# Kernel optimization log

Hardware: AMD Instinct MI355X
Metric: run time of the kernel (lower is better)

The kernel has to match this reference:

```python
import jax, jax.numpy as jnp
import numpy as np
import math

B, S, D, H = 2, 2048, 1024, 16
DH = D // H
EPS = 1e-5
GELU_C = 0.7978845608

def setup_inputs() -> dict:
    key = jax.random.key(0)
    ks = jax.random.split(key, 8)
    s = 0.02
    return {
        "x": jax.random.normal(ks[0], (B, S, D), jnp.float32),
        "gamma1": jnp.ones((D,), jnp.float32),
        "beta1": jnp.zeros((D,), jnp.float32),
        "W_qkv": jax.random.normal(ks[1], (D, 3 * D), jnp.float32) * s,
        "b_qkv": jnp.zeros((3 * D,), jnp.float32),
        "W_o": jax.random.normal(ks[2], (D, D), jnp.float32) * s,
        "b_o": jnp.zeros((D,), jnp.float32),
        "gamma2": jnp.ones((D,), jnp.float32),
        "beta2": jnp.zeros((D,), jnp.float32),
        "W_up": jax.random.normal(ks[3], (D, 4 * D), jnp.float32) * s,
        "b_up": jnp.zeros((4 * D,), jnp.float32),
        "W_down": jax.random.normal(ks[4], (4 * D, D), jnp.float32) * s,
        "b_down": jnp.zeros((D,), jnp.float32),
    }

def _layernorm(x, gamma, beta):
    # Matches the torch module: unbiased std (ddof=1), eps added to std.
    mean = jnp.mean(x, axis=-1, keepdims=True)
    std = jnp.std(x, axis=-1, keepdims=True, ddof=1)
    return gamma * (x - mean) / (std + EPS) + beta

def _gelu(x):
    return 0.5 * x * (1.0 + jnp.tanh(GELU_C * (x + 0.044715 * x * x * x)))

def reference(x, gamma1, beta1, W_qkv, b_qkv, W_o, b_o, gamma2, beta2, W_up, b_up, W_down, b_down):
    b, s, _ = x.shape
    # --- attention branch ---
    h = _layernorm(x, gamma1, beta1)
    qkv = (h @ W_qkv + b_qkv).reshape(b, s, H, 3, DH)
    q, k, v = qkv[..., 0, :], qkv[..., 1, :], qkv[..., 2, :]  # [b,s,h,dh]
    scores = jnp.einsum("bqhd,bkhd->bhqk", q, k) / math.sqrt(DH)
    causal = jnp.tril(jnp.ones((s, s), bool))
    scores = jnp.where(causal, scores, -jnp.inf)
    attn = jax.nn.softmax(scores, axis=-1)
    o = jnp.einsum("bhqk,bkhd->bqhd", attn, v).reshape(b, s, D)
    attn_out = o @ W_o + b_o + x
    # --- mlp branch ---
    h2 = _layernorm(attn_out, gamma2, beta2)
    mlp = _gelu(h2 @ W_up + b_up) @ W_down + b_down
    return mlp + attn_out
```

## Files before the change

### kernel.cpp

```cpp
#include <hip/hip_runtime.h>
#include <hip/hip_bf16.h>
#include <stdint.h>

constexpr int TS = 2048;
constexpr int TD = 1024;
constexpr int TM = 4096;
constexpr float GELU_C = 0.7978845608f;

typedef __hip_bfloat16 bf16;
typedef __attribute__((ext_vector_type(8))) short bf16x8;
typedef __attribute__((ext_vector_type(4))) float f32x4;
typedef __attribute__((ext_vector_type(16))) float f32x16;

__device__ __forceinline__ void gload16(const void* g, void* l) {
  __builtin_amdgcn_global_load_lds(
      (const __attribute__((address_space(1))) void*)g,
      (__attribute__((address_space(3))) void*)l, 16, 0, 0);
}

__device__ __forceinline__ unsigned short f2bfbits(float f) {
  bf16 h = __float2bfloat16(f);
  unsigned short u;
  __builtin_memcpy(&u, &h, 2);
  return u;
}

__device__ __forceinline__ uint32_t cvtpk_bf16(float lo, float hi) {
  uint32_t r;
  asm("v_cvt_pk_bf16_f32 %0, %1, %2" : "=v"(r) : "v"(lo), "v"(hi));
  return r;
}
__device__ __forceinline__ float ex2(float x) {
  float r;
  asm("v_exp_f32 %0, %1" : "=v"(r) : "v"(x));
  return r;
}

__device__ __forceinline__ float gelu_f(float x) {
  float x3 = x * x * x;
  return 0.5f * x * (1.0f + tanhf(GELU_C * (x + 0.044715f * x3)));
}

__global__ __launch_bounds__(256) void k_transpose_bf16(
    const float* __restrict__ W, bf16* __restrict__ Wt, int K, int N) {
  __shared__ float t[64][65];
  int k0 = blockIdx.x * 64, n0 = blockIdx.y * 64;
  int tid = threadIdx.x;
  int c = tid & 63, r0 = tid >> 6;
#pragma unroll
  for (int i = 0; i < 16; ++i) {
    int r = r0 + i * 4;
    t[r][c] = W[(size_t)(k0 + r) * N + n0 + c];
  }
  __syncthreads();
#pragma unroll
  for (int i = 0; i < 16; ++i) {
    int r = r0 + i * 4;
    Wt[(size_t)(n0 + r) * K + k0 + c] = __float2bfloat16(t[c][r]);
  }
}

__global__ __launch_bounds__(256) void k_layernorm(
    const float* __restrict__ x, const float* __restrict__ gamma,
    const float* __restrict__ beta, bf16* __restrict__ out) {
  int row = blockIdx.x;
  const float* xr = x + (size_t)row * TD;
  int tid = threadIdx.x;
  float4 v = ((const float4*)xr)[tid];
  float s = v.x + v.y + v.z + v.w;
  float ss = v.x * v.x + v.y * v.y + v.z * v.z + v.w * v.w;
#pragma unroll
  for (int off = 32; off; off >>= 1) {
    s += __shfl_down(s, off);
    ss += __shfl_down(ss, off);
  }
  __shared__ float red[8];
  __shared__ float stat[2];
  int wid = tid >> 6, lane = tid & 63;
  if (lane == 0) { red[wid] = s; red[4 + wid] = ss; }
  __syncthreads();
  if (tid == 0) {
    float S1 = red[0] + red[1] + red[2] + red[3];
    float S2 = red[4] + red[5] + red[6] + red[7];
    float mean = S1 / (float)TD;
    float var = (S2 - S1 * mean) / (float)(TD - 1);
    var = fmaxf(var, 0.0f);
    stat[0] = mean;
    stat[1] = 1.0f / (sqrtf(var) + 1e-5f);
  }
  __syncthreads();
  float mean = stat[0], rstd = stat[1];
  float4 g = ((const float4*)gamma)[tid];
  float4 bb = ((const float4*)beta)[tid];
  ushort4 r4;
  r4.x = f2bfbits(g.x * (v.x - mean) * rstd + bb.x);
  r4.y = f2bfbits(g.y * (v.y - mean) * rstd + bb.y);
  r4.z = f2bfbits(g.z * (v.z - mean) * rstd + bb.z);
  r4.w = f2bfbits(g.w * (v.w - mean) * rstd + bb.w);
  ((ushort4*)(out + (size_t)row * TD))[tid] = r4;
}

template <int MODE>
__global__ __launch_bounds__(256) void k_gemm(
    const bf16* __restrict__ A, const bf16* __restrict__ Bt,
    const float* __restrict__ bias, const float* __restrict__ resid,
    void* __restrict__ out, int Mm, int Nn, int Kk) {
  __shared__ __align__(1024) char smem[32768];
  char* sA = smem;
  char* sB = smem + 16384;
  int bm = blockIdx.y, bn = blockIdx.x;
  int tid = threadIdx.x, w = tid >> 6, lane = tid & 63;
  int wm = w >> 1, wn = w & 1;
  f32x4 acc[4][4] = {};
  size_t arow0 = (size_t)bm * 128;
  size_t brow0 = (size_t)bn * 128;
  int srow = lane >> 3;
  int sslot = (lane & 7) ^ srow;
  int nkt = Kk >> 6;
  for (int kt = 0; kt < nkt; ++kt) {
    __syncthreads();
#pragma unroll
    for (int t = 0; t < 4; ++t) {
      int chunk = w * 4 + t;
      int row = chunk * 8 + srow;
      const char* g = (const char*)(A + (arow0 + row) * (size_t)Kk + kt * 64) + sslot * 16;
      gload16(g, sA + chunk * 1024);
    }
#pragma unroll
    for (int t = 0; t < 4; ++t) {
      int chunk = w * 4 + t;
      int row = chunk * 8 + srow;
      const char* g = (const char*)(Bt + (brow0 + row) * (size_t)Kk + kt * 64) + sslot * 16;
      gload16(g, sB + chunk * 1024);
    }
    __syncthreads();
#pragma unroll
    for (int ks = 0; ks < 2; ++ks) {
      bf16x8 af[4], bfr[4];
#pragma unroll
      for (int i = 0; i < 4; ++i) {
        int row = wm * 64 + i * 16 + (lane & 15);
        int off = row * 128 + ((ks * 64 + (lane >> 4) * 16) ^ ((row & 7) << 4));
        af[i] = *(const bf16x8*)(sA + off);
      }
#pragma unroll
      for (int j = 0; j < 4; ++j) {
        int row = wn * 64 + j * 16 + (lane & 15);
        int off = row * 128 + ((ks * 64 + (lane >> 4) * 16) ^ ((row & 7) << 4));
        bfr[j] = *(const bf16x8*)(sB + off);
      }
#pragma unroll
      for (int i = 0; i < 4; ++i)
#pragma unroll
        for (int j = 0; j < 4; ++j)
          acc[i][j] = __builtin_amdgcn_mfma_f32_16x16x32_bf16(af[i], bfr[j], acc[i][j], 0, 0, 0);
    }
  }
  int rbase = (lane >> 4) * 4;
  int cbase = lane & 15;
#pragma unroll
  for (int i = 0; i < 4; ++i) {
#pragma unroll
    for (int j = 0; j < 4; ++j) {
      int n = bn * 128 + wn * 64 + j * 16 + cbase;
      float bv = bias[n];
#pragma unroll
      for (int r = 0; r < 4; ++r) {
        int m = bm * 128 + wm * 64 + i * 16 + rbase + r;
        float vv = acc[i][j][r] + bv;
        size_t idx = (size_t)m * Nn + n;
        if constexpr (MODE == 0) {
          ((bf16*)out)[idx] = __float2bfloat16(vv);
        } else if constexpr (MODE == 1) {
          ((float*)out)[idx] = vv + resid[idx];
        } else {
          ((bf16*)out)[idx] = __float2bfloat16(gelu_f(vv));
        }
      }
    }
  }
}

__global__ __launch_bounds__(256, 4) void k_attn(
    const bf16* __restrict__ qkv, bf16* __restrict__ outp) {
  int bh = blockIdx.x;
  int b = bh >> 4, hd = bh & 15;
  int T = 31 - (int)blockIdx.y;
  int tid = threadIdx.x, w = tid >> 6, lane = tid & 63;
  int qsub = w >> 1, ntw = w & 1;
  int ql = lane & 31;
  int half = lane >> 5;
  __shared__ __align__(1024) char smem[32768];
  char* sK0 = smem;
  char* sV0 = smem + 16384;
  const unsigned short* qkv_u =
      (const unsigned short*)(qkv + (size_t)b * TS * 3072 + hd * 192);
  int srowK = lane >> 3;
  int sslotK = (lane & 7) ^ srowK;
  constexpr float SCL = 0.18033688011f;

  int q0 = T * 64 + qsub * 32;
  int nkt = T + 1;
  int qlim = qsub * 32 + ql;

  const unsigned short* qrow = qkv_u + (size_t)(q0 + ql) * 3072;
  bf16x8 qf[4];
#pragma unroll
  for (int ks = 0; ks < 4; ++ks)
    qf[ks] = *(const bf16x8*)(qrow + ks * 16 + 8 * half);

  float m_st = -3.0e38f, l_own = 0.0f;
  f32x16 oaccT[2];
#pragma unroll
  for (int dt = 0; dt < 2; ++dt)
#pragma unroll
    for (int r = 0; r < 16; ++r) oaccT[dt][r] = 0.0f;

  uint32_t vr[16];

#define STAGE_K(KT, BUF)                                                      \
  {                                                                           \
    _Pragma("unroll")                                                         \
    for (int tt = 0; tt < 2; ++tt) {                                          \
      int chunk = w * 2 + tt;                                                 \
      int row = (KT) * 64 + chunk * 8 + srowK;                                \
      const char* g = (const char*)qkv_u + (size_t)row * 6144 + 128 +         \
                      sslotK * 16;                                            \
      gload16(g, sK0 + (BUF) * 8192 + chunk * 1024);                          \
    }                                                                         \
  }
#define LOAD_V(KT)                                                            \
  {                                                                           \
    _Pragma("unroll")                                                         \
    for (int p = 0; p < 16; ++p)                                              \
      vr[p] = qkv_u[(size_t)((KT) * 64 + w * 16 + p) * 3072 + 128 + lane];    \
  }
#define COMMIT_V(BUF)                                                         \
  {                                                                           \
    uint32_t wd[8];                                                           \
    _Pragma("unroll")                                                         \
    for (int e = 0; e < 8; ++e) wd[e] = vr[2 * e] | (vr[2 * e + 1] << 16);    \
    _Pragma("unroll")                                                         \
    for (int u = 0; u < 2; ++u) {                                             \
      uint4 q4;                                                               \
      q4.x = wd[4 * u]; q4.y = wd[4 * u + 1];                                 \
      q4.z = wd[4 * u + 2]; q4.w = wd[4 * u + 3];                             \
      int off = lane * 128 + ((w * 32 + u * 16) ^ ((lane & 7) << 4));         \
      *(uint4*)(sV0 + (BUF) * 8192 + off) = q4;                               \
    }                                                                         \
  }

  STAGE_K(0, 0);
  LOAD_V(0);
  COMMIT_V(0);
  __syncthreads();

  for (int kt = 0; kt < nkt; ++kt) {
    int cur = kt & 1;
    int nxt = cur ^ 1;
    if (kt + 1 < nkt) {
      STAGE_K(kt + 1, nxt);
      LOAD_V(kt + 1);
    }
    bool act = (kt < T) | (ntw <= qsub);
    if (act) {
      f32x16 sc;
#pragma unroll
      for (int r = 0; r < 16; ++r) sc[r] = 0.0f;
#pragma unroll
      for (int ks = 0; ks < 4; ++ks) {
        int row = ntw * 32 + ql;
        int off = row * 128 + ((ks * 32 + 16 * half) ^ ((row & 7) << 4));
        bf16x8 kf = *(const bf16x8*)(sK0 + cur * 8192 + off);
        sc = __builtin_amdgcn_mfma_f32_32x32x16_bf16(kf, qf[ks], sc, 0, 0, 0);
      }
      if (kt == T) {
#pragma unroll
        for (int r = 0; r < 16; ++r) {
          int loc = ntw * 32 + (r & 3) + 8 * (r >> 2) + 4 * half;
          float s = sc[r] * SCL;
          sc[r] = (loc <= qlim) ? s : -3.0e38f;
        }
      } else {
#pragma unroll
        for (int r = 0; r < 16; ++r) sc[r] *= SCL;
      }
      float t8[8];
#pragma unroll
      for (int e = 0; e < 8; ++e) t8[e] = fmaxf(sc[e], sc[e + 8]);
#pragma unroll
      for (int e = 0; e < 4; ++e) t8[e] = fmaxf(t8[e], t8[e + 4]);
      float pm = fmaxf(fmaxf(t8[0], t8[2]), fmaxf(t8[1], t8[3]));
      pm = fmaxf(pm, __shfl_xor(pm, 32));
      if (!__all(pm <= m_st + 11.5f)) {
        float mn = fmaxf(m_st, pm);
        float f = ex2(m_st - mn);
        l_own *= f;
#pragma unroll
        for (int dt = 0; dt < 2; ++dt)
#pragma unroll
          for (int r = 0; r < 16; ++r) oaccT[dt][r] *= f;
        m_st = mn;
      }
#pragma unroll
      for (int r = 0; r < 16; ++r) sc[r] = ex2(sc[r] - m_st);
#pragma unroll
      for (int e = 0; e < 8; ++e) t8[e] = sc[e] + sc[e + 8];
#pragma unroll
      for (int e = 0; e < 4; ++e) t8[e] = t8[e] + t8[e + 4];
      l_own += (t8[0] + t8[2]) + (t8[1] + t8[3]);
      uint32_t w8[8];
#pragma unroll
      for (int g = 0; g < 4; ++g)
#pragma unroll
        for (int e = 0; e < 2; ++e)
          w8[g * 2 + e] = cvtpk_bf16(sc[4 * g + 2 * e], sc[4 * g + 2 * e + 1]);
      uint32_t rcv[2][2];
#pragma unroll
      for (int s = 0; s < 2; ++s)
#pragma unroll
        for (int e = 0; e < 2; ++e) {
          uint32_t snd = half ? w8[4 * s + e] : w8[4 * s + 2 + e];
          rcv[s][e] = (uint32_t)__shfl_xor((int)snd, 32);
        }
#pragma unroll
      for (int s = 0; s < 2; ++s) {
        union { uint32_t u[4]; bf16x8 v; } pf;
        if (half == 0) {
          pf.u[0] = w8[4 * s]; pf.u[1] = w8[4 * s + 1];
          pf.u[2] = rcv[s][0]; pf.u[3] = rcv[s][1];
        } else {
          pf.u[0] = rcv[s][0]; pf.u[1] = rcv[s][1];
          pf.u[2] = w8[4 * s + 2]; pf.u[3] = w8[4 * s + 3];
        }
#pragma unroll
        for (int dt = 0; dt < 2; ++dt) {
          int row = dt * 32 + ql;
          int off = row * 128 +
                    ((ntw * 64 + s * 32 + 16 * half) ^ ((row & 7) << 4));
          bf16x8 vtf = *(const bf16x8*)(sV0 + cur * 8192 + off);
          oaccT[dt] = __builtin_amdgcn_mfma_f32_32x32x16_bf16(vtf, pf.v, oaccT[dt], 0, 0, 0);
        }
      }
    }
    if (kt + 1 < nkt) COMMIT_V(nxt);
    __syncthreads();
  }

  float l_tot = l_own + __shfl_xor(l_own, 32);
  float* scr = (float*)smem;
  if (ntw == 1) {
    scr[(0 * 2 + qsub) * 64 + lane] = m_st;
    scr[(1 * 2 + qsub) * 64 + lane] = l_tot;
#pragma unroll
    for (int dt = 0; dt < 2; ++dt)
#pragma unroll
      for (int r = 0; r < 16; ++r)
        scr[((2 + dt * 16 + r) * 2 + qsub) * 64 + lane] = oaccT[dt][r];
  }
  __syncthreads();
  if (ntw == 0) {
    float mB = scr[(0 * 2 + qsub) * 64 + lane];
    float lB = scr[(1 * 2 + qsub) * 64 + lane];
    float m = fmaxf(m_st, mB);
    float wa = ex2(m_st - m), wb = ex2(mB - m);
    float linv = 1.0f / (l_tot * wa + lB * wb);
    int qg = q0 + ql;
    bf16* orow = outp + (size_t)(b * TS + qg) * TD + hd * 64;
#pragma unroll
    for (int dt = 0; dt < 2; ++dt)
#pragma unroll
      for (int g = 0; g < 4; ++g) {
        ushort4 s4;
        float o0, o1, o2, o3;
        o0 = (oaccT[dt][4 * g] * wa +
              scr[((2 + dt * 16 + 4 * g) * 2 + qsub) * 64 + lane] * wb) * linv;
        o1 = (oaccT[dt][4 * g + 1] * wa +
              scr[((2 + dt * 16 + 4 * g + 1) * 2 + qsub) * 64 + lane] * wb) * linv;
        o2 = (oaccT[dt][4 * g + 2] * wa +
              scr[((2 + dt * 16 + 4 * g + 2) * 2 + qsub) * 64 + lane] * wb) * linv;
        o3 = (oaccT[dt][4 * g + 3] * wa +
              scr[((2 + dt * 16 + 4 * g + 3) * 2 + qsub) * 64 + lane] * wb) * linv;
        s4.x = f2bfbits(o0); s4.y = f2bfbits(o1);
        s4.z = f2bfbits(o2); s4.w = f2bfbits(o3);
        *(ushort4*)(orow + dt * 32 + 8 * g + 4 * half) = s4;
      }
  }
#undef STAGE_K
#undef LOAD_V
#undef COMMIT_V
}

extern "C" void kernel_launch(void* const* d_in, const int* in_sizes, int n_in,
                              void* d_out, int out_size, void* d_ws, size_t ws_size,
                              hipStream_t stream) {
  const float* x      = (const float*)d_in[0];
  const float* gamma1 = (const float*)d_in[1];
  const float* beta1  = (const float*)d_in[2];
  const float* W_qkv  = (const float*)d_in[3];
  const float* b_qkv  = (const float*)d_in[4];
  const float* W_o    = (const float*)d_in[5];
  const float* b_o    = (const float*)d_in[6];
  const float* gamma2 = (const float*)d_in[7];
  const float* beta2  = (const float*)d_in[8];
  const float* W_up   = (const float*)d_in[9];
  const float* b_up   = (const float*)d_in[10];
  const float* W_down = (const float*)d_in[11];
  const float* b_down = (const float*)d_in[12];

  char* ws = (char*)d_ws;
  bf16*  wt_qkv  = (bf16*)(ws + 0);
  bf16*  wt_o    = (bf16*)(ws + 6291456);
  bf16*  wt_up   = (bf16*)(ws + 8388608);
  bf16*  wt_down = (bf16*)(ws + 16777216);
  bf16*  h1      = (bf16*)(ws + 25165824);
  bf16*  qkvb    = (bf16*)(ws + 33554432);
  bf16*  ob      = (bf16*)(ws + 58720256);
  float* attn_o  = (float*)(ws + 67108864);
  bf16*  h2      = (bf16*)(ws + 83886080);
  bf16*  ub      = (bf16*)(ws + 92274688);
  float* outf    = (float*)d_out;

  k_transpose_bf16<<<dim3(16, 48), 256, 0, stream>>>(W_qkv, wt_qkv, 1024, 3072);
  k_transpose_bf16<<<dim3(16, 16), 256, 0, stream>>>(W_o, wt_o, 1024, 1024);
  k_transpose_bf16<<<dim3(16, 64), 256, 0, stream>>>(W_up, wt_up, 1024, 4096);
  k_transpose_bf16<<<dim3(64, 16), 256, 0, stream>>>(W_down, wt_down, 4096, 1024);

  k_layernorm<<<TM, 256, 0, stream>>>(x, gamma1, beta1, h1);
  k_gemm<0><<<dim3(24, 32), 256, 0, stream>>>(h1, wt_qkv, b_qkv, nullptr, qkvb, TM, 3072, 1024);
  k_attn<<<dim3(32, 32), 256, 0, stream>>>(qkvb, ob);
  k_gemm<1><<<dim3(8, 32), 256, 0, stream>>>(ob, wt_o, b_o, x, attn_o, TM, 1024, 1024);
  k_layernorm<<<TM, 256, 0, stream>>>(attn_o, gamma2, beta2, h2);
  k_gemm<2><<<dim3(32, 32), 256, 0, stream>>>(h2, wt_up, b_up, nullptr, ub, TM, 4096, 1024);
  k_gemm<1><<<dim3(8, 32), 256, 0, stream>>>(ub, wt_down, b_down, attn_o, outf, TM, 1024, 4096);
}
```

Measured before the change: 372.7 us.

## Add BM-templated GEMM tiles, XCD-aware block swizzle, and exp2-based GELU

Templates the GEMM on row-tile height so the two N=1024 GEMMs use 64x128 tiles, giving 512 blocks instead of 256 to fill the 256 CUs better. Blocks now launch on a 1D grid and are remapped with a stride-8 swizzle so neighbouring tiles share XCD caches. GELU's tanhf is replaced with an exp2-based tanh expression, which is cheaper but may lose a little accuracy or overflow for large inputs (e→inf gives th=1, which is fine). Smaller tiles reduce per-block reuse of the B operand.

```diff
diff --git a/kernel.cpp b/kernel.cpp
--- a/kernel.cpp
+++ b/kernel.cpp
@@ -37,8 +37,10 @@
 }
 
 __device__ __forceinline__ float gelu_f(float x) {
-  float x3 = x * x * x;
-  return 0.5f * x * (1.0f + tanhf(GELU_C * (x + 0.044715f * x3)));
+  float u = GELU_C * (x + 0.044715f * x * x * x);
+  float e = ex2(u * 2.8853900818f);
+  float th = 1.0f - 2.0f / (e + 1.0f);
+  return 0.5f * x * (1.0f + th);
 }
 
 __global__ __launch_bounds__(256) void k_transpose_bf16(
@@ -100,19 +102,29 @@
   ((ushort4*)(out + (size_t)row * TD))[tid] = r4;
 }
 
-template <int MODE>
+template <int MODE, int BM>
 __global__ __launch_bounds__(256) void k_gemm(
     const bf16* __restrict__ A, const bf16* __restrict__ Bt,
     const float* __restrict__ bias, const float* __restrict__ resid,
-    void* __restrict__ out, int Mm, int Nn, int Kk) {
-  __shared__ __align__(1024) char smem[32768];
+    void* __restrict__ out, int Nn, int Kk) {
+  constexpr int NBM = TM / BM;
+  constexpr int WN = (BM == 128) ? 2 : 4;
+  constexpr int WTN = 128 / WN;
+  constexpr int NJ = WTN / 16;
+  constexpr int TA = BM / 32;
+  __shared__ __align__(1024) char smem[BM * 128 + 16384];
   char* sA = smem;
-  char* sB = smem + 16384;
-  int bm = blockIdx.y, bn = blockIdx.x;
+  char* sB = smem + BM * 128;
+  int total = gridDim.x;
+  int orig = blockIdx.x;
+  int swz = (orig & 7) * (total >> 3) + (orig >> 3);
+  int bm = swz & (NBM - 1);
+  int bn = swz / NBM;
   int tid = threadIdx.x, w = tid >> 6, lane = tid & 63;
-  int wm = w >> 1, wn = w & 1;
-  f32x4 acc[4][4] = {};
-  size_t arow0 = (size_t)bm * 128;
+  int wm = (BM == 128) ? (w >> 1) : 0;
+  int wn = (BM == 128) ? (w & 1) : w;
+  f32x4 acc[4][NJ] = {};
+  size_t arow0 = (size_t)bm * BM;
   size_t brow0 = (size_t)bn * 128;
   int srow = lane >> 3;
   int sslot = (lane & 7) ^ srow;
@@ -120,8 +132,8 @@
   for (int kt = 0; kt < nkt; ++kt) {
     __syncthreads();
 #pragma unroll
-    for (int t = 0; t < 4; ++t) {
-      int chunk = w * 4 + t;
+    for (int t = 0; t < TA; ++t) {
+      int chunk = w * TA + t;
       int row = chunk * 8 + srow;
       const char* g = (const char*)(A + (arow0 + row) * (size_t)Kk + kt * 64) + sslot * 16;
       gload16(g, sA + chunk * 1024);
@@ -136,7 +148,7 @@
     __syncthreads();
 #pragma unroll
     for (int ks = 0; ks < 2; ++ks) {
-      bf16x8 af[4], bfr[4];
+      bf16x8 af[4], bfr[NJ];
 #pragma unroll
       for (int i = 0; i < 4; ++i) {
         int row = wm * 64 + i * 16 + (lane & 15);
@@ -144,15 +156,15 @@
         af[i] = *(const bf16x8*)(sA + off);
       }
 #pragma unroll
-      for (int j = 0; j < 4; ++j) {
-        int row = wn * 64 + j * 16 + (lane & 15);
+      for (int j = 0; j < NJ; ++j) {
+        int row = wn * WTN + j * 16 + (lane & 15);
         int off = row * 128 + ((ks * 64 + (lane >> 4) * 16) ^ ((row & 7) << 4));
         bfr[j] = *(const bf16x8*)(sB + off);
       }
 #pragma unroll
       for (int i = 0; i < 4; ++i)
 #pragma unroll
-        for (int j = 0; j < 4; ++j)
+        for (int j = 0; j < NJ; ++j)
           acc[i][j] = __builtin_amdgcn_mfma_f32_16x16x32_bf16(af[i], bfr[j], acc[i][j], 0, 0, 0);
     }
   }
@@ -161,12 +173,12 @@
 #pragma unroll
   for (int i = 0; i < 4; ++i) {
 #pragma unroll
-    for (int j = 0; j < 4; ++j) {
-      int n = bn * 128 + wn * 64 + j * 16 + cbase;
+    for (int j = 0; j < NJ; ++j) {
+      int n = bn * 128 + wn * WTN + j * 16 + cbase;
       float bv = bias[n];
 #pragma unroll
       for (int r = 0; r < 4; ++r) {
-        int m = bm * 128 + wm * 64 + i * 16 + rbase + r;
+        int m = bm * BM + wm * 64 + i * 16 + rbase + r;
         float vv = acc[i][j][r] + bv;
         size_t idx = (size_t)m * Nn + n;
         if constexpr (MODE == 0) {
@@ -427,10 +439,10 @@
   k_transpose_bf16<<<dim3(64, 16), 256, 0, stream>>>(W_down, wt_down, 4096, 1024);
 
   k_layernorm<<<TM, 256, 0, stream>>>(x, gamma1, beta1, h1);
-  k_gemm<0><<<dim3(24, 32), 256, 0, stream>>>(h1, wt_qkv, b_qkv, nullptr, qkvb, TM, 3072, 1024);
+  k_gemm<0, 128><<<768, 256, 0, stream>>>(h1, wt_qkv, b_qkv, nullptr, qkvb, 3072, 1024);
   k_attn<<<dim3(32, 32), 256, 0, stream>>>(qkvb, ob);
-  k_gemm<1><<<dim3(8, 32), 256, 0, stream>>>(ob, wt_o, b_o, x, attn_o, TM, 1024, 1024);
+  k_gemm<1, 64><<<512, 256, 0, stream>>>(ob, wt_o, b_o, x, attn_o, 1024, 1024);
   k_layernorm<<<TM, 256, 0, stream>>>(attn_o, gamma2, beta2, h2);
-  k_gemm<2><<<dim3(32, 32), 256, 0, stream>>>(h2, wt_up, b_up, nullptr, ub, TM, 4096, 1024);
-  k_gemm<1><<<dim3(8, 32), 256, 0, stream>>>(ub, wt_down, b_down, attn_o, outf, TM, 1024, 4096);
-}
+  k_gemm<2, 128><<<1024, 256, 0, stream>>>(h2, wt_up, b_up, nullptr, ub, 4096, 1024);
+  k_gemm<1, 64><<<512, 256, 0, stream>>>(ub, wt_down, b_down, attn_o, outf, 1024, 4096);
+}
```

Result: faster. 347.4 us (-6.8%).
